# Performance work log

Measured on AMD Instinct MI355X. Metric: run time of the kernel, lower is better.

Reference implementation:

```python
import jax, jax.numpy as jnp
import numpy as np

D_MODEL = 1024
N_HEADS = 16
D_EXP = 4
B, SQ, SKV = 2, 2048, 2048
LN_EPS = 1e-5


def _linear_params(key, d_in, d_out):
    kw, kb = jax.random.split(key)
    w = jax.random.normal(kw, (d_in, d_out), jnp.float32) * 0.02  # stored [in,out]
    b = jax.random.normal(kb, (d_out,), jnp.float32) * 0.02
    return w, b


def setup_inputs() -> dict:
    key = jax.random.key(0)
    ks = jax.random.split(key, 16)
    inp = {}
    inp["x"] = jax.random.normal(ks[0], (B, SQ, D_MODEL), jnp.float32)
    inp["encoder_out"] = jax.random.normal(ks[1], (B, SKV, D_MODEL), jnp.float32)
    # causal target mask, broadcast over batch and heads
    inp["tgt_mask"] = jnp.tril(jnp.ones((SQ, SQ), jnp.int32))[None, None]
    inp["src_mask"] = jnp.ones((1, 1, SQ, SKV), jnp.int32)
    # self-attention params
    inp["wq_s"], inp["bq_s"] = _linear_params(ks[2], D_MODEL, D_MODEL)
    inp["wk_s"], inp["bk_s"] = _linear_params(ks[3], D_MODEL, D_MODEL)
    inp["wv_s"], inp["bv_s"] = _linear_params(ks[4], D_MODEL, D_MODEL)
    inp["wo_s"], inp["bo_s"] = _linear_params(ks[5], D_MODEL, D_MODEL)
    # cross-attention params
    inp["wq_c"], inp["bq_c"] = _linear_params(ks[6], D_MODEL, D_MODEL)
    inp["wk_c"], inp["bk_c"] = _linear_params(ks[7], D_MODEL, D_MODEL)
    inp["wv_c"], inp["bv_c"] = _linear_params(ks[8], D_MODEL, D_MODEL)
    inp["wo_c"], inp["bo_c"] = _linear_params(ks[9], D_MODEL, D_MODEL)
    # feedforward params
    inp["ff1_w"], inp["ff1_b"] = _linear_params(ks[10], D_MODEL, D_MODEL * D_EXP)
    inp["ff2_w"], inp["ff2_b"] = _linear_params(ks[11], D_MODEL * D_EXP, D_MODEL)
    # layernorm params (3 AddNorms)
    for i, k in zip((1, 2, 3), (ks[12], ks[13], ks[14])):
        inp[f"ln{i}_g"] = jnp.ones((D_MODEL,), jnp.float32)
        inp[f"ln{i}_b"] = jnp.zeros((D_MODEL,), jnp.float32)
    return inp


def _layernorm(x, g, b):
    mu = jnp.mean(x, axis=-1, keepdims=True)
    var = jnp.mean(jnp.square(x - mu), axis=-1, keepdims=True)
    return (x - mu) / jnp.sqrt(var + LN_EPS) * g + b


def _mha(xq, xkv, wq, bq, wk, bk, wv, bv, wo, bo, mask):
    Bq, Sq, D = xq.shape
    Hd = D // N_HEADS
    q = (xq @ wq + bq).reshape(Bq, Sq, N_HEADS, Hd).transpose(0, 2, 1, 3)   # bhqd
    k = (xkv @ wk + bk).reshape(Bq, -1, N_HEADS, Hd).transpose(0, 2, 1, 3)  # bhkd
    v = (xkv @ wv + bv).reshape(Bq, -1, N_HEADS, Hd).transpose(0, 2, 1, 3)  # bhkd
    score = jnp.einsum("bhqd,bhkd->bhqk", q, k) / jnp.sqrt(jnp.float32(Hd))
    score = jnp.where(mask == 0, -jnp.inf, score)
    attn = jax.nn.softmax(score, axis=-1)
    ctx = jnp.einsum("bhqk,bhkd->bhqd", attn, v)
    ctx = ctx.transpose(0, 2, 1, 3).reshape(Bq, Sq, D)
    return ctx @ wo + bo


def reference(x, encoder_out, tgt_mask, src_mask,
              wq_s, bq_s, wk_s, bk_s, wv_s, bv_s, wo_s, bo_s,
              wq_c, bq_c, wk_c, bk_c, wv_c, bv_c, wo_c, bo_c,
              ff1_w, ff1_b, ff2_w, ff2_b,
              ln1_g, ln1_b, ln2_g, ln2_b, ln3_g, ln3_b):
    # dropout is identity in eval mode
    sa = _mha(x, x, wq_s, bq_s, wk_s, bk_s, wv_s, bv_s, wo_s, bo_s, tgt_mask)
    h = _layernorm(x + sa, ln1_g, ln1_b)
    ca = _mha(h, encoder_out, wq_c, bq_c, wk_c, bk_c, wv_c, bv_c, wo_c, bo_c, src_mask)
    h2 = _layernorm(h + ca, ln2_g, ln2_b)
    ff = jax.nn.relu(h2 @ ff1_w + ff1_b) @ ff2_w + ff2_b
    return _layernorm(h2 + ff, ln3_g, ln3_b)
```

## Files before the change

### kernel.cpp

```cpp
#include <hip/hip_runtime.h>
#include <stdint.h>

typedef __bf16 bf16;
typedef __attribute__((ext_vector_type(4))) float f32x4;
typedef __attribute__((ext_vector_type(8))) __bf16 bf16x8;
typedef __attribute__((ext_vector_type(4))) __bf16 bf16x4;
typedef __attribute__((ext_vector_type(4))) short s16x4;

#define DM   1024
#define NH   16
#define HDIM 64
#define BB   2
#define SEQ  2048
#define MR   (BB * SEQ)
#define DFF  4096
#define MEG  (1024 * 1024)

__global__ void detect_kernel(const unsigned int* __restrict__ xw,
                              int* __restrict__ flag) {
  int tid = threadIdx.x;
  int bad = 0;
  for (int i = tid; i < 4096; i += 64) {
    unsigned int w = xw[i];
    float flo = __uint_as_float((w & 0xffffu) << 16);
    if (!(fabsf(flo) < 100.f)) bad = 1;
  }
  unsigned long long m = __ballot(bad);
  if (tid == 0) *flag = (m == 0ull) ? 1 : 0;
}

__global__ __launch_bounds__(256) void cvt_big_kernel(
    const void* __restrict__ src, bf16* __restrict__ dst, int n4,
    const int* __restrict__ flag) {
  int i = blockIdx.x * 256 + threadIdx.x;
  if (i >= n4) return;
  if (*flag) {
    ((bf16x4*)dst)[i] = ((const bf16x4*)src)[i];
  } else {
    float4 v = ((const float4*)src)[i];
    bf16x4 o = {(bf16)v.x, (bf16)v.y, (bf16)v.z, (bf16)v.w};
    ((bf16x4*)dst)[i] = o;
  }
}

struct P16 { const void* p[16]; };
__global__ __launch_bounds__(256) void cvt_small_kernel(
    P16 ps, bf16* __restrict__ dstbase, const int* __restrict__ flag) {
  const int ncnt[16] = {1024,1024,1024,1024,1024,1024,1024,1024,
                        4096,1024,1024,1024,1024,1024,1024,1024};
  const int doff[16] = {0,1024,2048,3072,4096,5120,6144,7168,
                        8192,12288,13312,14336,15360,16384,17408,18432};
  int b = blockIdx.x;
  int n = ncnt[b];
  bool isbf = (*flag) != 0;
  const void* s = ps.p[b];
  bf16* d = dstbase + doff[b];
  for (int i = threadIdx.x; i * 4 < n; i += 256) {
    if (isbf) {
      ((bf16x4*)d)[i] = ((const bf16x4*)s)[i];
    } else {
      float4 v = ((const float4*)s)[i];
      bf16x4 o = {(bf16)v.x, (bf16)v.y, (bf16)v.z, (bf16)v.w};
      ((bf16x4*)d)[i] = o;
    }
  }
}

static __device__ __forceinline__ void gl_lds16(const bf16* g, bf16* l) {
  auto gp = reinterpret_cast<__attribute__((address_space(1))) unsigned int*>(
      reinterpret_cast<uintptr_t>(g));
  auto lp = reinterpret_cast<__attribute__((address_space(3))) unsigned int*>(
      (unsigned int)reinterpret_cast<uintptr_t>(l));
  __builtin_amdgcn_global_load_lds(gp, lp, 16, 0, 0);
}

static __device__ __forceinline__ s16x4 as_s16x4(bf16x4 v) {
  s16x4 r;
  __builtin_memcpy(&r, &v, 8);
  return r;
}

struct WTB {
  const void* src[10];
  int dstoff[10];
  int K[10], N[10];
  int bstart[10];
};
__global__ __launch_bounds__(256) void wt_all_kernel(WTB wb, bf16* __restrict__ wtbase,
                                                     const int* __restrict__ flag) {
  __shared__ bf16 tile[32][33];
  int bid = blockIdx.x;
  int wi = 0;
  while (wi < 9 && bid >= wb.bstart[wi + 1]) ++wi;
  int rel = bid - wb.bstart[wi];
  int N = wb.N[wi], K = wb.K[wi];
  int nb = N >> 5;
  int n0 = (rel % nb) * 32, k0 = (rel / nb) * 32;
  const void* w = wb.src[wi];
  bf16* wt = wtbase + wb.dstoff[wi];
  bool isbf = (*flag) != 0;
  int tid = threadIdx.x;
  int tx = tid & 31, ty = tid >> 5;
#pragma unroll
  for (int i = 0; i < 4; ++i) {
    size_t idx = (size_t)(k0 + ty + i * 8) * N + n0 + tx;
    tile[ty + i * 8][tx] = isbf ? ((const bf16*)w)[idx]
                                : (bf16)(((const float*)w)[idx]);
  }
  __syncthreads();
#pragma unroll
  for (int i = 0; i < 4; ++i)
    wt[(size_t)(n0 + ty + i * 8) * K + k0 + tx] = tile[tx][ty + i * 8];
}

template <int TM>
__global__ __launch_bounds__(256) void gemm_kernel(
    const bf16* __restrict__ A, const bf16* __restrict__ Bt,
    const bf16* __restrict__ bias, bf16* __restrict__ outb,
    int M, int N, int K, int relu) {
  constexpr int NI = TM / 32;
  constexpr int WM = TM / 2;
  constexpr int CA = TM / 64;
  __shared__ alignas(16) bf16 As[TM * 32];
  __shared__ alignas(16) bf16 Bs[128 * 32];
  int tid = threadIdx.x;
  int lane = tid & 63, wv = tid >> 6;
  int quad = lane >> 4, l15 = lane & 15;
  int m0 = blockIdx.y * TM, n0 = blockIdx.x * 128;
  int wm = wv >> 1, wn = wv & 1;

  f32x4 acc[NI][4];
#pragma unroll
  for (int i = 0; i < NI; ++i)
#pragma unroll
    for (int j = 0; j < 4; ++j) acc[i][j] = (f32x4){0.f, 0.f, 0.f, 0.f};

  int sr = lane >> 2, sc = (lane & 3) * 8;
  const bf16* gA[CA];
  bf16* lA[CA];
#pragma unroll
  for (int t = 0; t < CA; ++t) {
    int ch = wv * CA + t;
    gA[t] = A + (size_t)(m0 + ch * 16 + sr) * K + sc;
    lA[t] = As + ch * 512 + lane * 8;
  }
  const bf16* gB0 = Bt + (size_t)(n0 + (wv * 2) * 16 + sr) * K + sc;
  const bf16* gB1 = Bt + (size_t)(n0 + (wv * 2 + 1) * 16 + sr) * K + sc;
  bf16* lB0 = Bs + (wv * 2) * 512 + lane * 8;
  bf16* lB1 = Bs + (wv * 2 + 1) * 512 + lane * 8;

  for (int k0 = 0; k0 < K; k0 += 32) {
#pragma unroll
    for (int t = 0; t < CA; ++t) gl_lds16(gA[t] + k0, lA[t]);
    gl_lds16(gB0 + k0, lB0);
    gl_lds16(gB1 + k0, lB1);
    __syncthreads();
    bf16x8 af[NI], bfr[4];
#pragma unroll
    for (int i = 0; i < NI; ++i)
      af[i] = *(const bf16x8*)(As + (wm * WM + i * 16 + l15) * 32 + quad * 8);
#pragma unroll
    for (int j = 0; j < 4; ++j)
      bfr[j] = *(const bf16x8*)(Bs + (wn * 64 + j * 16 + l15) * 32 + quad * 8);
#pragma unroll
    for (int i = 0; i < NI; ++i)
#pragma unroll
      for (int j = 0; j < 4; ++j)
        acc[i][j] = __builtin_amdgcn_mfma_f32_16x16x32_bf16(af[i], bfr[j],
                                                            acc[i][j], 0, 0, 0);
    __syncthreads();
  }

#pragma unroll
  for (int j = 0; j < 4; ++j) {
    int col = n0 + wn * 64 + j * 16 + l15;
    float bval = (float)bias[col];
#pragma unroll
    for (int i = 0; i < NI; ++i) {
      int rb = m0 + wm * WM + i * 16 + quad * 4;
#pragma unroll
      for (int r = 0; r < 4; ++r) {
        float v = acc[i][j][r] + bval;
        if (relu) v = fmaxf(v, 0.f);
        outb[(size_t)(rb + r) * N + col] = (bf16)v;
      }
    }
  }
}

__global__ __launch_bounds__(256) void gemm_splitk_kernel(
    const bf16* __restrict__ A, const bf16* __restrict__ Bt,
    float* __restrict__ pout, int M, int N, int KC, int Ktot) {
  __shared__ alignas(16) bf16 As[128 * 32];
  __shared__ alignas(16) bf16 Bs[128 * 32];
  int tid = threadIdx.x;
  int lane = tid & 63, wv = tid >> 6;
  int quad = lane >> 4, l15 = lane & 15;
  int m0 = blockIdx.y * 128, n0 = blockIdx.x * 128;
  int wm = wv >> 1, wn = wv & 1;
  int kb = blockIdx.z * KC;
  pout += (size_t)blockIdx.z * M * N;

  f32x4 acc[4][4];
#pragma unroll
  for (int i = 0; i < 4; ++i)
#pragma unroll
    for (int j = 0; j < 4; ++j) acc[i][j] = (f32x4){0.f, 0.f, 0.f, 0.f};

  int sr = lane >> 2, sc = (lane & 3) * 8;
  const bf16* gA0 = A + (size_t)(m0 + (wv * 2) * 16 + sr) * Ktot + sc;
  const bf16* gA1 = A + (size_t)(m0 + (wv * 2 + 1) * 16 + sr) * Ktot + sc;
  const bf16* gB0 = Bt + (size_t)(n0 + (wv * 2) * 16 + sr) * Ktot + sc;
  const bf16* gB1 = Bt + (size_t)(n0 + (wv * 2 + 1) * 16 + sr) * Ktot + sc;
  bf16* lA0 = As + (wv * 2) * 512 + lane * 8;
  bf16* lA1 = As + (wv * 2 + 1) * 512 + lane * 8;
  bf16* lB0 = Bs + (wv * 2) * 512 + lane * 8;
  bf16* lB1 = Bs + (wv * 2 + 1) * 512 + lane * 8;

  for (int k0 = kb; k0 < kb + KC; k0 += 32) {
    gl_lds16(gA0 + k0, lA0);
    gl_lds16(gA1 + k0, lA1);
    gl_lds16(gB0 + k0, lB0);
    gl_lds16(gB1 + k0, lB1);
    __syncthreads();
    bf16x8 af[4], bfr[4];
#pragma unroll
    for (int i = 0; i < 4; ++i)
      af[i] = *(const bf16x8*)(As + (wm * 64 + i * 16 + l15) * 32 + quad * 8);
#pragma unroll
    for (int j = 0; j < 4; ++j)
      bfr[j] = *(const bf16x8*)(Bs + (wn * 64 + j * 16 + l15) * 32 + quad * 8);
#pragma unroll
    for (int i = 0; i < 4; ++i)
#pragma unroll
      for (int j = 0; j < 4; ++j)
        acc[i][j] = __builtin_amdgcn_mfma_f32_16x16x32_bf16(af[i], bfr[j],
                                                            acc[i][j], 0, 0, 0);
    __syncthreads();
  }
#pragma unroll
  for (int j = 0; j < 4; ++j) {
    int col = n0 + wn * 64 + j * 16 + l15;
#pragma unroll
    for (int i = 0; i < 4; ++i) {
      int rb = m0 + wm * 64 + i * 16 + quad * 4;
#pragma unroll
      for (int r = 0; r < 4; ++r)
        pout[(size_t)(rb + r) * N + col] = acc[i][j][r];
    }
  }
}

__global__ __launch_bounds__(256) void vt_pre_kernel(
    const bf16* __restrict__ v, int vstride, bf16* __restrict__ vt, int skv) {
  __shared__ bf16 tile[32][33];
  int tid = threadIdx.x;
  int tx = tid & 31, ty = tid >> 5;
  int kv0 = blockIdx.x * 32, d0 = blockIdx.y * 32;
  int bh = blockIdx.z;
  int b = bh >> 4, h = bh & 15;
  const bf16* src = v + (size_t)b * skv * vstride + h * HDIM;
#pragma unroll
  for (int i = 0; i < 4; ++i)
    tile[ty + i * 8][tx] = src[(size_t)(kv0 + ty + i * 8) * vstride + d0 + tx];
  __syncthreads();
  bf16* dst = vt + ((size_t)bh * HDIM + d0) * skv + kv0;
#pragma unroll
  for (int i = 0; i < 4; ++i)
    dst[(size_t)(ty + i * 8) * skv + tx] = tile[tx][ty + i * 8];
}

__global__ __launch_bounds__(256, 4) void flash8_kernel(
    const bf16* __restrict__ Q, int qstride,
    const bf16* __restrict__ Kk, int kstride,
    const bf16* __restrict__ VT, bf16* __restrict__ ctx,
    float* __restrict__ opart, float* __restrict__ lpart,
    int skv, int causal, int nsplit) {
  __shared__ alignas(16) bf16 KTl[2][64 * 64];
  __shared__ alignas(16) bf16 VTl[2][64 * 64];
  int tid = threadIdx.x;
  int lane = tid & 63, wv = tid >> 6, quad = lane >> 4, l15 = lane & 15;
  int qb = blockIdx.x, h = blockIdx.y;
  int zz = blockIdx.z;
  int b = zz / nsplit;
  int half = zz - b * nsplit;
  int q0 = qb * 128;
  int qw = q0 + wv * 32;
  int l7 = l15 & 7;

  bf16x8 qf[2][2];
  const float qsc = 0.125f * 1.44269504f;
#pragma unroll
  for (int a = 0; a < 2; ++a) {
    const bf16* qp = Q + (size_t)(b * SEQ + qw + a * 16 + l15) * qstride + h * HDIM;
    qf[a][0] = *(const bf16x8*)(qp + quad * 8);
    qf[a][1] = *(const bf16x8*)(qp + 32 + quad * 8);
#pragma unroll
    for (int j = 0; j < 8; ++j) {
      qf[a][0][j] = (bf16)((float)qf[a][0][j] * qsc);
      qf[a][1][j] = (bf16)((float)qf[a][1][j] * qsc);
    }
  }
  s16x4 onesA = {0x3F80, 0x3F80, 0x3F80, 0x3F80};

  f32x4 o[2][4], oL[2];
#pragma unroll
  for (int a = 0; a < 2; ++a) {
    oL[a] = (f32x4){0.f, 0.f, 0.f, 0.f};
#pragma unroll
    for (int j = 0; j < 4; ++j) o[a][j] = (f32x4){0.f, 0.f, 0.f, 0.f};
  }

  int nch_tot = causal ? (q0 + 128) / 64 : skv / 64;
  int c_lo = (half * nch_tot) / nsplit;
  int c_hi = ((half + 1) * nch_tot) / nsplit;

  int l8 = lane >> 3;
  int colseg = (lane & 7) ^ l8;
  int grow = wv * 16 + l8;
  const bf16* kbase = Kk + ((size_t)b * skv + grow) * kstride + h * HDIM + colseg * 8;
  const bf16* vbase = VT + ((size_t)(b * NH + h) * HDIM + grow) * skv + colseg * 8;
  bf16* kls = &KTl[0][wv * 1024];
  bf16* vls = &VTl[0][wv * 1024];

  auto STAGE = [&](int bb, int cc) {
    const bf16* ks = kbase + (size_t)(cc * 64) * kstride;
    const bf16* vs = vbase + cc * 64;
    bf16* kd = kls + bb * 4096;
    bf16* vd = vls + bb * 4096;
    gl_lds16(ks, kd);
    gl_lds16(ks + (size_t)8 * kstride, kd + 512);
    gl_lds16(vs, vd);
    gl_lds16(vs + (size_t)8 * skv, vd + 512);
  };

  if (c_lo < c_hi) STAGE(0, c_lo);

  for (int c = c_lo; c < c_hi; ++c) {
    int cur = (c - c_lo) & 1;
    int kv0 = c * 64;
    __syncthreads();
    if (c + 1 < c_hi) STAGE(cur ^ 1, c + 1);

    if (!causal || kv0 <= qw + 31) {
      const bf16* kt_base = &KTl[0][0] + cur * 4096;
      const bf16* vt_base = &VTl[0][0] + cur * 4096;
      bf16x4 p[2][4];
#pragma unroll
      for (int t = 0; t < 4; ++t) {
        const bf16* kb = kt_base + (t * 16 + l15) * 64;
        bf16x8 kt0 = *(const bf16x8*)(kb + ((quad ^ l7) << 3));
        bf16x8 kt1 = *(const bf16x8*)(kb + (((quad + 4) ^ l7) << 3));
#pragma unroll
        for (int a = 0; a < 2; ++a) {
          f32x4 z = (f32x4){0.f, 0.f, 0.f, 0.f};
          z = __builtin_amdgcn_mfma_f32_16x16x32_bf16(kt0, qf[a][0], z, 0, 0, 0);
          z = __builtin_amdgcn_mfma_f32_16x16x32_bf16(kt1, qf[a][1], z, 0, 0, 0);
          if (causal && kv0 + 63 > qw) {
#pragma unroll
            for (int r = 0; r < 4; ++r)
              if (kv0 + t * 16 + quad * 4 + r > qw + a * 16 + l15)
                z[r] = -1e30f;
          }
          bf16x4 pk;
#pragma unroll
          for (int r = 0; r < 4; ++r) pk[r] = (bf16)exp2f(z[r]);
          p[a][t] = pk;
          oL[a] = __builtin_amdgcn_mfma_f32_16x16x16bf16_1k(
              onesA, as_s16x4(pk), oL[a], 0, 0, 0);
        }
      }
#pragma unroll
      for (int jt = 0; jt < 4; ++jt) {
        const bf16* vb = vt_base + (jt * 16 + l15) * 64;
        bf16x4 af[4];
#pragma unroll
        for (int t = 0; t < 4; ++t)
          af[t] = *(const bf16x4*)(
              vb + ((((t * 2 + (quad >> 1)) ^ l7) << 3) + ((quad & 1) << 2)));
#pragma unroll
        for (int a = 0; a < 2; ++a)
#pragma unroll
          for (int t = 0; t < 4; ++t)
            o[a][jt] = __builtin_amdgcn_mfma_f32_16x16x16bf16_1k(
                as_s16x4(af[t]), as_s16x4(p[a][t]), o[a][jt], 0, 0, 0);
      }
    }
  }

  if (nsplit == 1) {
#pragma unroll
    for (int a = 0; a < 2; ++a) {
      float inv = 1.0f / fmaxf(oL[a][0], 1e-30f);
      bf16* cp = ctx + (size_t)(b * SEQ + qw + a * 16 + l15) * DM + h * HDIM + quad * 4;
#pragma unroll
      for (int jt = 0; jt < 4; ++jt) {
        bf16x4 ob = {(bf16)(o[a][jt][0] * inv), (bf16)(o[a][jt][1] * inv),
                     (bf16)(o[a][jt][2] * inv), (bf16)(o[a][jt][3] * inv)};
        *(bf16x4*)(cp + jt * 16) = ob;
      }
    }
  } else {
#pragma unroll
    for (int a = 0; a < 2; ++a) {
      float* op = opart + (size_t)half * MR * DM +
                  (size_t)(b * SEQ + qw + a * 16 + l15) * DM + h * HDIM + quad * 4;
#pragma unroll
      for (int jt = 0; jt < 4; ++jt) *(f32x4*)(op + jt * 16) = o[a][jt];
      if (lane < 16)
        lpart[(size_t)((half * BB + b) * NH + h) * SEQ + qw + a * 16 + l15] =
            oL[a][0];
    }
  }
}

template <int NS>
__global__ __launch_bounds__(256) void flash_comb_kernel(
    const float* __restrict__ opart, const float* __restrict__ lpart,
    bf16* __restrict__ ctx) {
  int row = blockIdx.x, tid = threadIdx.x;
  int b = row >> 11, q = row & (SEQ - 1);
  int h = tid >> 4;
  float l = 0.f;
#pragma unroll
  for (int s = 0; s < NS; ++s)
    l += lpart[(size_t)((s * BB + b) * NH + h) * SEQ + q];
  float inv = 1.0f / fmaxf(l, 1e-30f);
  float a0 = 0.f, a1 = 0.f, a2 = 0.f, a3 = 0.f;
#pragma unroll
  for (int s = 0; s < NS; ++s) {
    f32x4 v = ((const f32x4*)(opart + (size_t)s * MR * DM + (size_t)row * DM))[tid];
    a0 += v[0]; a1 += v[1]; a2 += v[2]; a3 += v[3];
  }
  bf16x4 ob = {(bf16)(a0 * inv), (bf16)(a1 * inv),
               (bf16)(a2 * inv), (bf16)(a3 * inv)};
  ((bf16x4*)(ctx + (size_t)row * DM))[tid] = ob;
}

template <int NP>
__global__ __launch_bounds__(256) void addnorm_red_kernel(
    const bf16* __restrict__ res, const float* __restrict__ part,
    const bf16* __restrict__ bias, const bf16* __restrict__ g,
    const bf16* __restrict__ be, bf16* __restrict__ yb,
    void* __restrict__ outAny, const int* __restrict__ flag) {
  int row = blockIdx.x, tid = threadIdx.x;
  float a0 = 0.f, a1 = 0.f, a2 = 0.f, a3 = 0.f;
#pragma unroll
  for (int p = 0; p < NP; ++p) {
    float4 v = ((const float4*)(part + (size_t)p * MR * DM + (size_t)row * DM))[tid];
    a0 += v.x; a1 += v.y; a2 += v.z; a3 += v.w;
  }
  bf16x4 bb = ((const bf16x4*)bias)[tid];
  bf16x4 rr = ((const bf16x4*)(res + (size_t)row * DM))[tid];
  float s0 = (float)rr[0] + a0 + (float)bb[0];
  float s1 = (float)rr[1] + a1 + (float)bb[1];
  float s2 = (float)rr[2] + a2 + (float)bb[2];
  float s3 = (float)rr[3] + a3 + (float)bb[3];
  float sum = s0 + s1 + s2 + s3;
  float sq = s0 * s0 + s1 * s1 + s2 * s2 + s3 * s3;
#pragma unroll
  for (int mk = 32; mk >= 1; mk >>= 1) {
    sum += __shfl_xor(sum, mk, 64);
    sq += __shfl_xor(sq, mk, 64);
  }
  __shared__ float red[8];
  int wvi = tid >> 6, lane = tid & 63;
  if (lane == 0) { red[wvi * 2] = sum; red[wvi * 2 + 1] = sq; }
  __syncthreads();
  sum = red[0] + red[2] + red[4] + red[6];
  sq = red[1] + red[3] + red[5] + red[7];
  float mu = sum * (1.0f / DM);
  float var = sq * (1.0f / DM) - mu * mu;
  float rstd = rsqrtf(var + 1e-5f);
  bf16x4 g4 = ((const bf16x4*)g)[tid];
  bf16x4 b4 = ((const bf16x4*)be)[tid];
  float y0 = (s0 - mu) * rstd * (float)g4[0] + (float)b4[0];
  float y1 = (s1 - mu) * rstd * (float)g4[1] + (float)b4[1];
  float y2 = (s2 - mu) * rstd * (float)g4[2] + (float)b4[2];
  float y3 = (s3 - mu) * rstd * (float)g4[3] + (float)b4[3];
  if (yb) {
    bf16x4 ob = {(bf16)y0, (bf16)y1, (bf16)y2, (bf16)y3};
    ((bf16x4*)(yb + (size_t)row * DM))[tid] = ob;
  }
  if (outAny) {
    if (*flag) {
      bf16x4 ob = {(bf16)y0, (bf16)y1, (bf16)y2, (bf16)y3};
      ((bf16x4*)outAny)[(size_t)row * 256 + tid] = ob;
    } else {
      ((float4*)outAny)[(size_t)row * 256 + tid] = make_float4(y0, y1, y2, y3);
    }
  }
}

extern "C" void kernel_launch(void* const* d_in, const int* in_sizes, int n_in,
                              void* d_out, int out_size, void* d_ws, size_t ws_size,
                              hipStream_t stream) {
  (void)in_sizes; (void)n_in; (void)out_size; (void)ws_size;
  const void* x_raw   = d_in[0];
  const void* enc_raw = d_in[1];

  char* ws = (char*)d_ws;
  size_t off = 0;
  auto alloc = [&](size_t bytes) -> void* {
    void* p = ws + off;
    off += (bytes + 255) & ~(size_t)255;
    return p;
  };
  const size_t SB = (size_t)MR * DM;
  int* flag    = (int*)alloc(256);
  bf16* smallb = (bf16*)alloc(20480 * 2);
  bf16* wt   = (bf16*)alloc((size_t)16 * MEG * 2);
  bf16* xb   = (bf16*)alloc(SB * 2);
  bf16* encb = (bf16*)alloc(SB * 2);
  bf16* vtg  = (bf16*)alloc(SB * 2);
  bf16* ctx  = (bf16*)alloc(SB * 2);
  bf16* hb1  = (bf16*)alloc(SB * 2);
  bf16* hb2  = (bf16*)alloc(SB * 2);
  bf16* qkv  = (bf16*)alloc(SB * 3 * 2);
  bf16* kvc  = (bf16*)alloc(SB * 2 * 2);
  float* part = (float*)alloc(SB * 4 * 4);
  float* lpart = (float*)alloc((size_t)3 * BB * NH * SEQ * 4);
  bf16* gbuf = qkv;
  bf16* qc   = xb;

  bf16* b_qkvs = smallb + 0;     bf16* b_os  = smallb + 3072;
  bf16* b_qc   = smallb + 4096;  bf16* b_kvc = smallb + 5120;
  bf16* b_oc   = smallb + 7168;  bf16* b_f1  = smallb + 8192;
  bf16* b_f2   = smallb + 12288;
  bf16* l1g = smallb + 13312; bf16* l1b = smallb + 14336;
  bf16* l2g = smallb + 15360; bf16* l2b = smallb + 16384;
  bf16* l3g = smallb + 17408; bf16* l3b = smallb + 18432;

  detect_kernel<<<1, 64, 0, stream>>>((const unsigned int*)x_raw, flag);
  cvt_big_kernel<<<(int)(SB / 1024), 256, 0, stream>>>(x_raw, xb, (int)(SB / 4), flag);
  cvt_big_kernel<<<(int)(SB / 1024), 256, 0, stream>>>(enc_raw, encb, (int)(SB / 4), flag);
  P16 ps;
  ps.p[0] = d_in[5];  ps.p[1] = d_in[7];  ps.p[2] = d_in[9];  ps.p[3] = d_in[11];
  ps.p[4] = d_in[13]; ps.p[5] = d_in[15]; ps.p[6] = d_in[17]; ps.p[7] = d_in[19];
  ps.p[8] = d_in[21]; ps.p[9] = d_in[23];
  ps.p[10] = d_in[24]; ps.p[11] = d_in[25]; ps.p[12] = d_in[26];
  ps.p[13] = d_in[27]; ps.p[14] = d_in[28]; ps.p[15] = d_in[29];
  cvt_small_kernel<<<16, 256, 0, stream>>>(ps, smallb, flag);

  WTB wb;
  const int wsrc[10] = {4, 6, 8, 10, 12, 14, 16, 18, 20, 22};
  for (int i = 0; i < 10; ++i) {
    wb.src[i] = d_in[wsrc[i]];
    wb.K[i] = 1024; wb.N[i] = 1024;
    wb.dstoff[i] = i * MEG;
    wb.bstart[i] = i * 1024;
  }
  wb.N[8] = 4096;
  wb.K[9] = 4096; wb.dstoff[9] = 12 * MEG;
  wb.bstart[9] = 8192 + 4096;
  wt_all_kernel<<<16384, 256, 0, stream>>>(wb, wt, flag);

  gemm_kernel<128><<<dim3(24, 32), 256, 0, stream>>>(xb, wt, b_qkvs, qkv,
                                                     MR, 3072, DM, 0);
  vt_pre_kernel<<<dim3(SEQ / 32, 2, 32), 256, 0, stream>>>(qkv + 2048, 3072, vtg, SEQ);
  flash8_kernel<<<dim3(SEQ / 128, NH, BB * 2), 256, 0, stream>>>(
      qkv, 3072, qkv + 1024, 3072, vtg, ctx, part, lpart, SEQ, 1, 2);
  flash_comb_kernel<2><<<MR, 256, 0, stream>>>(part, lpart, ctx);
  gemm_splitk_kernel<<<dim3(8, 32, 2), 256, 0, stream>>>(
      ctx, wt + (size_t)3 * MEG, part, MR, DM, 512, DM);
  addnorm_red_kernel<2><<<MR, 256, 0, stream>>>(xb, part, b_os, l1g, l1b,
                                                hb1, nullptr, flag);
  gemm_kernel<64><<<dim3(8, 64), 256, 0, stream>>>(hb1, wt + (size_t)4 * MEG,
                                                   b_qc, qc, MR, DM, DM, 0);
  gemm_kernel<128><<<dim3(16, 32), 256, 0, stream>>>(encb, wt + (size_t)5 * MEG,
                                                     b_kvc, kvc, MR, 2048, DM, 0);
  vt_pre_kernel<<<dim3(SEQ / 32, 2, 32), 256, 0, stream>>>(kvc + 1024, 2048, vtg, SEQ);
  flash8_kernel<<<dim3(SEQ / 128, NH, BB), 256, 0, stream>>>(
      qc, 1024, kvc, 2048, vtg, ctx, nullptr, nullptr, SEQ, 0, 1);
  gemm_splitk_kernel<<<dim3(8, 32, 2), 256, 0, stream>>>(
      ctx, wt + (size_t)7 * MEG, part, MR, DM, 512, DM);
  addnorm_red_kernel<2><<<MR, 256, 0, stream>>>(hb1, part, b_oc, l2g, l2b,
                                                hb2, nullptr, flag);
  gemm_kernel<128><<<dim3(32, 32), 256, 0, stream>>>(hb2, wt + (size_t)8 * MEG,
                                                     b_f1, gbuf, MR, DFF, DM, 1);
  gemm_splitk_kernel<<<dim3(8, 32, 4), 256, 0, stream>>>(
      gbuf, wt + (size_t)12 * MEG, part, MR, DM, 1024, DFF);
  addnorm_red_kernel<4><<<MR, 256, 0, stream>>>(hb2, part, b_f2, l3g, l3b,
                                                nullptr, d_out, flag);
}
```

Measured before the change: 665.1 us.

## Vectorize weight transpose tiles and split cross-attention KV across two partitions

The weight transpose kernel now handles 64x32 tiles: each thread reads two adjacent elements and writes 16-byte vectors, which halves the block count and widens global stores. Cross-attention flash now runs with a 2-way KV split (doubling the grid) followed by the existing combine kernel, so more work runs in parallel on the GPU. In exchange it adds a combine pass and extra partial-buffer traffic. The LDS tile layout, padded to 40 columns, may cause bank conflicts on the strided writes.

Result: no change. 658.5 us (-1.0%).

```diff
diff --git a/kernel.cpp b/kernel.cpp
--- a/kernel.cpp
+++ b/kernel.cpp
@@ -88,29 +88,42 @@
 };
 __global__ __launch_bounds__(256) void wt_all_kernel(WTB wb, bf16* __restrict__ wtbase,
                                                      const int* __restrict__ flag) {
-  __shared__ bf16 tile[32][33];
+  __shared__ alignas(16) bf16 tile[64][40];
   int bid = blockIdx.x;
   int wi = 0;
   while (wi < 9 && bid >= wb.bstart[wi + 1]) ++wi;
   int rel = bid - wb.bstart[wi];
   int N = wb.N[wi], K = wb.K[wi];
-  int nb = N >> 5;
-  int n0 = (rel % nb) * 32, k0 = (rel / nb) * 32;
+  int nb = N >> 6;
+  int n0 = (rel % nb) * 64, k0 = (rel / nb) * 32;
   const void* w = wb.src[wi];
   bf16* wt = wtbase + wb.dstoff[wi];
   bool isbf = (*flag) != 0;
   int tid = threadIdx.x;
-  int tx = tid & 31, ty = tid >> 5;
+  int np = tid & 31, tk = tid >> 5;
 #pragma unroll
   for (int i = 0; i < 4; ++i) {
-    size_t idx = (size_t)(k0 + ty + i * 8) * N + n0 + tx;
-    tile[ty + i * 8][tx] = isbf ? ((const bf16*)w)[idx]
-                                : (bf16)(((const float*)w)[idx]);
+    int kl = tk + i * 8;
+    bf16 b0, b1;
+    if (isbf) {
+      unsigned int u = *(const unsigned int*)(
+          (const bf16*)w + (size_t)(k0 + kl) * N + n0 + np * 2);
+      unsigned short s0 = (unsigned short)(u & 0xffffu);
+      unsigned short s1 = (unsigned short)(u >> 16);
+      __builtin_memcpy(&b0, &s0, 2);
+      __builtin_memcpy(&b1, &s1, 2);
+    } else {
+      const float* fp = (const float*)w + (size_t)(k0 + kl) * N + n0 + np * 2;
+      b0 = (bf16)fp[0];
+      b1 = (bf16)fp[1];
+    }
+    tile[np * 2][kl] = b0;
+    tile[np * 2 + 1][kl] = b1;
   }
   __syncthreads();
-#pragma unroll
-  for (int i = 0; i < 4; ++i)
-    wt[(size_t)(n0 + ty + i * 8) * K + k0 + tx] = tile[tx][ty + i * 8];
+  int nl = tid >> 2, kq = tid & 3;
+  bf16x8 v = *(const bf16x8*)(&tile[nl][kq * 8]);
+  *(bf16x8*)(wt + (size_t)(n0 + nl) * K + k0 + kq * 8) = v;
 }
 
 template <int TM>
@@ -544,16 +557,22 @@
 
   WTB wb;
   const int wsrc[10] = {4, 6, 8, 10, 12, 14, 16, 18, 20, 22};
+  int bacc = 0;
   for (int i = 0; i < 10; ++i) {
     wb.src[i] = d_in[wsrc[i]];
     wb.K[i] = 1024; wb.N[i] = 1024;
     wb.dstoff[i] = i * MEG;
-    wb.bstart[i] = i * 1024;
+    wb.bstart[i] = bacc;
+    bacc += (1024 / 64) * (1024 / 32);
   }
   wb.N[8] = 4096;
   wb.K[9] = 4096; wb.dstoff[9] = 12 * MEG;
-  wb.bstart[9] = 8192 + 4096;
-  wt_all_kernel<<<16384, 256, 0, stream>>>(wb, wt, flag);
+  bacc = 0;
+  for (int i = 0; i < 10; ++i) {
+    wb.bstart[i] = bacc;
+    bacc += (wb.N[i] / 64) * (wb.K[i] / 32);
+  }
+  wt_all_kernel<<<bacc, 256, 0, stream>>>(wb, wt, flag);
 
   gemm_kernel<128><<<dim3(24, 32), 256, 0, stream>>>(xb, wt, b_qkvs, qkv,
                                                      MR, 3072, DM, 0);
@@ -570,8 +589,9 @@
   gemm_kernel<128><<<dim3(16, 32), 256, 0, stream>>>(encb, wt + (size_t)5 * MEG,
                                                      b_kvc, kvc, MR, 2048, DM, 0);
   vt_pre_kernel<<<dim3(SEQ / 32, 2, 32), 256, 0, stream>>>(kvc + 1024, 2048, vtg, SEQ);
-  flash8_kernel<<<dim3(SEQ / 128, NH, BB), 256, 0, stream>>>(
-      qc, 1024, kvc, 2048, vtg, ctx, nullptr, nullptr, SEQ, 0, 1);
+  flash8_kernel<<<dim3(SEQ / 128, NH, BB * 2), 256, 0, stream>>>(
+      qc, 1024, kvc, 2048, vtg, ctx, part, lpart, SEQ, 0, 2);
+  flash_comb_kernel<2><<<MR, 256, 0, stream>>>(part, lpart, ctx);
   gemm_splitk_kernel<<<dim3(8, 32, 2), 256, 0, stream>>>(
       ctx, wt + (size_t)7 * MEG, part, MR, DM, 512, DM);
   addnorm_red_kernel<2><<<MR, 256, 0, stream>>>(hb1, part, b_oc, l2g, l2b,
```
